# Optimization experiments

Measured on AMD Instinct MI355X. Metric: run time of the kernel, lower is better.

The kernel has to match this reference:

```python
import jax, jax.numpy as jnp
import numpy as np

N_NODES = 50000
N_EDGES = 800000
IN_DIM = 128
HIDDEN = 256
N_CLASSES = 10
N_GRAPHS = 64


def setup_inputs() -> dict:
    key = jax.random.key(0)
    ks = jax.random.split(key, 12)
    x = jax.random.normal(ks[0], (N_NODES, IN_DIM), dtype=jnp.float32)
    edge_index = jax.random.randint(ks[1], (2, N_EDGES), 0, N_NODES, dtype=jnp.int64)
    batch = jnp.sort(jax.random.randint(ks[2], (N_NODES,), 0, N_GRAPHS, dtype=jnp.int64))
    s = 1.0 / np.sqrt(IN_DIM)
    sh = 1.0 / np.sqrt(HIDDEN)
    return {
        "x": x,
        "edge_index": edge_index,
        "batch": batch,
        # layer 0 (in_dim -> hidden), weights stored [in, out]
        "Wg0": jax.random.uniform(ks[3], (IN_DIM, HIDDEN), jnp.float32, -s, s),
        "Wl0": jax.random.uniform(ks[4], (IN_DIM, HIDDEN), jnp.float32, -s, s),
        "Ws0": jax.random.uniform(ks[5], (IN_DIM, HIDDEN), jnp.float32, -s, s),
        "b0": jnp.zeros((HIDDEN,), jnp.float32),
        # layer 1 (hidden -> hidden)
        "Wg1": jax.random.uniform(ks[6], (HIDDEN, HIDDEN), jnp.float32, -sh, sh),
        "Wl1": jax.random.uniform(ks[7], (HIDDEN, HIDDEN), jnp.float32, -sh, sh),
        "Ws1": jax.random.uniform(ks[8], (HIDDEN, HIDDEN), jnp.float32, -sh, sh),
        "b1": jnp.zeros((HIDDEN,), jnp.float32),
        # classifier (hidden -> num_classes)
        "Wc": jax.random.uniform(ks[9], (HIDDEN, N_CLASSES), jnp.float32, -sh, sh),
        "bc": jax.random.uniform(ks[10], (N_CLASSES,), jnp.float32, -sh, sh),
    }


def _demo_layer(h, src, dst, deg, Wg, Wl, Ws, b):
    # global transform on all nodes
    g = h @ Wg
    # per-node mean of neighbor features over outgoing edges (== degree-bucket mean)
    neigh_sum = jax.ops.segment_sum(h[dst], src, num_segments=N_NODES)
    neigh_mean = neigh_sum / jnp.maximum(deg, 1.0)[:, None]
    # degree-0 nodes receive only the global branch (as in the torch loop)
    out = g + jnp.where((deg > 0)[:, None], neigh_mean @ Wl + h @ Ws, 0.0)
    return jax.nn.elu(out + b)  # dropout is identity in eval mode


def reference(x, edge_index, batch, Wg0, Wl0, Ws0, b0, Wg1, Wl1, Ws1, b1, Wc, bc):
    src, dst = edge_index[0], edge_index[1]
    deg = jax.ops.segment_sum(jnp.ones(src.shape[0], x.dtype), src, num_segments=N_NODES)
    h = _demo_layer(x, src, dst, deg, Wg0, Wl0, Ws0, b0)
    h = _demo_layer(h, src, dst, deg, Wg1, Wl1, Ws1, b1)
    # global mean pool per graph
    cnt = jax.ops.segment_sum(jnp.ones(N_NODES, h.dtype), batch, num_segments=N_GRAPHS)
    g = jax.ops.segment_sum(h, batch, num_segments=N_GRAPHS) / jnp.maximum(cnt, 1.0)[:, None]
    return g @ Wc + bc
```

## Files before the change

### kernel.cpp

```cpp
#include <hip/hip_runtime.h>

#define N_NODES 50000
#define N_PAD   50048
#define N_EDGES 800000
#define IN_DIM 128
#define HIDDEN 256
#define N_CLASSES 10
#define N_GRAPHS 64

#define SCAN_BLK 1024
#define NB_SCAN ((N_NODES + SCAN_BLK - 1) / SCAN_BLK)

typedef __attribute__((ext_vector_type(8))) short short8;
typedef __attribute__((ext_vector_type(4))) float f32x4;

__device__ __forceinline__ float bf2f(unsigned short h) {
    union { unsigned int u; float f; } v; v.u = ((unsigned int)h) << 16; return v.f;
}
__device__ __forceinline__ unsigned short f2bf(float f) {
    union { float f; unsigned int u; } v; v.f = f;
    unsigned int u = v.u;
    u += 0x7FFFu + ((u >> 16) & 1u);
    return (unsigned short)(u >> 16);
}

__global__ void deg_count_kernel(const int* __restrict__ src, int* __restrict__ deg) {
    int e = blockIdx.x * blockDim.x + threadIdx.x;
    if (e < N_EDGES) atomicAdd(&deg[src[e]], 1);
}

__global__ __launch_bounds__(SCAN_BLK)
void block_sum_kernel(const int* __restrict__ deg, int* __restrict__ blocksum) {
    __shared__ int red[SCAN_BLK / 64];
    int i = blockIdx.x * SCAN_BLK + threadIdx.x;
    int v = (i < N_NODES) ? deg[i] : 0;
    #pragma unroll
    for (int off = 32; off; off >>= 1) v += __shfl_down(v, off, 64);
    if ((threadIdx.x & 63) == 0) red[threadIdx.x >> 6] = v;
    __syncthreads();
    if (threadIdx.x < 64) {
        int s = (threadIdx.x < SCAN_BLK / 64) ? red[threadIdx.x] : 0;
        #pragma unroll
        for (int off = 8; off; off >>= 1) s += __shfl_down(s, off, 64);
        if (threadIdx.x == 0) blocksum[blockIdx.x] = s;
    }
}

__global__ void block_offset_kernel(const int* __restrict__ blocksum, int* __restrict__ blockoff) {
    int lane = threadIdx.x;
    int v = (lane < NB_SCAN) ? blocksum[lane] : 0;
    #pragma unroll
    for (int off = 1; off < 64; off <<= 1) {
        int t = __shfl_up(v, off, 64);
        if (lane >= off) v += t;
    }
    int ex = __shfl_up(v, 1, 64);
    if (lane == 0) ex = 0;
    if (lane < NB_SCAN) blockoff[lane] = ex;
}

__global__ __launch_bounds__(SCAN_BLK)
void scan_phase_c_kernel(const int* __restrict__ deg, const int* __restrict__ blockoff,
                         int* __restrict__ rowptr, int* __restrict__ cursor,
                         float* __restrict__ rdeg,
                         int* __restrict__ d0cnt, int* __restrict__ d0list) {
    __shared__ int buf[SCAN_BLK];
    int i = blockIdx.x * SCAN_BLK + threadIdx.x;
    int v = (i < N_NODES) ? deg[i] : 0;
    buf[threadIdx.x] = v;
    __syncthreads();
    #pragma unroll
    for (int off = 1; off < SCAN_BLK; off <<= 1) {
        int t = (threadIdx.x >= off) ? buf[threadIdx.x - off] : 0;
        __syncthreads();
        buf[threadIdx.x] += t;
        __syncthreads();
    }
    int incl = buf[threadIdx.x] + blockoff[blockIdx.x];
    if (i < N_NODES) {
        rowptr[i + 1] = incl;
        cursor[i] = incl - v;
        rdeg[i] = (v > 0) ? 1.0f / (float)v : 0.0f;
        if (v == 0) { int p = atomicAdd(d0cnt, 1); d0list[p] = i; }
        if (i == 0) rowptr[0] = 0;
    }
}

__global__ void csr_fill_kernel(const int* __restrict__ src, const int* __restrict__ dst,
                                int* __restrict__ cursor, int* __restrict__ csr) {
    int e = blockIdx.x * blockDim.x + threadIdx.x;
    if (e < N_EDGES) {
        int p = atomicAdd(&cursor[src[e]], 1);
        csr[p] = dst[e];
    }
}

__global__ void cvt_bf16_kernel(const float* __restrict__ in, unsigned short* __restrict__ out, int n4) {
    int i = blockIdx.x * blockDim.x + threadIdx.x;
    if (i >= n4) return;
    float4 v = reinterpret_cast<const float4*>(in)[i];
    ushort4 o;
    o.x = f2bf(v.x); o.y = f2bf(v.y); o.z = f2bf(v.z); o.w = f2bf(v.w);
    reinterpret_cast<ushort4*>(out)[i] = o;
}

template<int D>
__global__ void prep_w_kernel(const float* __restrict__ Wg, const float* __restrict__ Wl,
                              const float* __restrict__ Ws, unsigned short* __restrict__ Wt) {
    int i = blockIdx.x * blockDim.x + threadIdx.x;
    if (i >= 256 * 2 * D) return;
    int c = i / (2 * D), k = i % (2 * D);
    float v;
    if (k < D) v = Wg[(size_t)k * 256 + c] + Ws[(size_t)k * 256 + c];
    else       v = Wl[(size_t)(k - D) * 256 + c];
    Wt[i] = f2bf(v);
}

template<int D>
__global__ __launch_bounds__(256)
void gather_mean_kernel(const int* __restrict__ rowptr, const int* __restrict__ csr,
                        const float* __restrict__ rdeg,
                        const unsigned short* __restrict__ H, unsigned short* __restrict__ NS) {
    constexpr int LPR = D / 8;
    constexpr int EPW = 64 / LPR;
    int node = blockIdx.x * 4 + (threadIdx.x >> 6);
    if (node >= N_NODES) return;
    const int lane = threadIdx.x & 63;
    const int sub = lane / LPR;
    const int sl  = lane % LPR;
    const int lo = rowptr[node], hi = rowptr[node + 1];
    const uint4* H4 = reinterpret_cast<const uint4*>(H);
    float a0=0.f,a1=0.f,a2=0.f,a3=0.f,a4=0.f,a5=0.f,a6=0.f,a7=0.f;
#define ACC8(v)                                        \
    do {                                               \
        a0 += bf2f((v).x & 0xFFFF); a1 += bf2f((v).x >> 16); \
        a2 += bf2f((v).y & 0xFFFF); a3 += bf2f((v).y >> 16); \
        a4 += bf2f((v).z & 0xFFFF); a5 += bf2f((v).z >> 16); \
        a6 += bf2f((v).w & 0xFFFF); a7 += bf2f((v).w >> 16); \
    } while (0)
    int j = lo;
    for (; j + 4 * EPW <= hi; j += 4 * EPW) {
        int d0 = csr[j + 0 * EPW + sub];
        int d1 = csr[j + 1 * EPW + sub];
        int d2 = csr[j + 2 * EPW + sub];
        int d3 = csr[j + 3 * EPW + sub];
        uint4 v0 = H4[(size_t)d0 * LPR + sl];
        uint4 v1 = H4[(size_t)d1 * LPR + sl];
        uint4 v2 = H4[(size_t)d2 * LPR + sl];
        uint4 v3 = H4[(size_t)d3 * LPR + sl];
        ACC8(v0); ACC8(v1); ACC8(v2); ACC8(v3);
    }
    for (; j + sub < hi; j += EPW) {
        uint4 v0 = H4[(size_t)csr[j + sub] * LPR + sl];
        ACC8(v0);
    }
#undef ACC8
    #pragma unroll
    for (int off = LPR; off < 64; off <<= 1) {
        a0 += __shfl_xor(a0, off, 64);
        a1 += __shfl_xor(a1, off, 64);
        a2 += __shfl_xor(a2, off, 64);
        a3 += __shfl_xor(a3, off, 64);
        a4 += __shfl_xor(a4, off, 64);
        a5 += __shfl_xor(a5, off, 64);
        a6 += __shfl_xor(a6, off, 64);
        a7 += __shfl_xor(a7, off, 64);
    }
    if (sub == 0) {
        float r = rdeg[node];
        uint4 o;
        o.x = (unsigned int)f2bf(a0 * r) | ((unsigned int)f2bf(a1 * r) << 16);
        o.y = (unsigned int)f2bf(a2 * r) | ((unsigned int)f2bf(a3 * r) << 16);
        o.z = (unsigned int)f2bf(a4 * r) | ((unsigned int)f2bf(a5 * r) << 16);
        o.w = (unsigned int)f2bf(a6 * r) | ((unsigned int)f2bf(a7 * r) << 16);
        reinterpret_cast<uint4*>(NS)[(size_t)node * LPR + sl] = o;
    }
}

template<int D>
__global__ __launch_bounds__(512)
void gemm_mfma_kernel(const unsigned short* __restrict__ X, const unsigned short* __restrict__ NS,
                      const unsigned short* __restrict__ Wt, const float* __restrict__ bias,
                      unsigned short* __restrict__ OUT) {
    constexpr int KTOT = 2 * D;
    __shared__ __align__(16) unsigned short A_lds[128 * 64];
    __shared__ __align__(16) unsigned short B_lds[256 * 64];
    const int tid = threadIdx.x;
    const int lane = tid & 63;
    const int wid = tid >> 6;
    const int wm = wid >> 2, wn = wid & 3;
    const int rowbase = blockIdx.x * 128;

    f32x4 acc[4][4];
    #pragma unroll
    for (int i = 0; i < 4; ++i)
        #pragma unroll
        for (int j = 0; j < 4; ++j) acc[i][j] = (f32x4)0.0f;

    for (int kt = 0; kt < KTOT; kt += 64) {
        const unsigned short* Aseg = (kt < D) ? X : NS;
        const int kd0 = (kt < D) ? kt : kt - D;
        #pragma unroll
        for (int p = 0; p < 2; ++p) {
            int c = (p * 8 + wid) * 64 + lane;
            int row = c >> 3, sl = c & 7;
            int ss = sl ^ (row & 7);
            const unsigned short* g = Aseg + (size_t)(rowbase + row) * D + kd0 + ss * 8;
            unsigned short* l = &A_lds[(size_t)(p * 8 + wid) * 512];
            __builtin_amdgcn_global_load_lds((const __attribute__((address_space(1))) unsigned int*)g,
                                             (__attribute__((address_space(3))) unsigned int*)l, 16, 0, 0);
        }
        #pragma unroll
        for (int p = 0; p < 4; ++p) {
            int c = (p * 8 + wid) * 64 + lane;
            int br = c >> 3, sl = c & 7;
            int ss = sl ^ (br & 7);
            const unsigned short* g = Wt + (size_t)br * KTOT + kt + ss * 8;
            unsigned short* l = &B_lds[(size_t)(p * 8 + wid) * 512];
            __builtin_amdgcn_global_load_lds((const __attribute__((address_space(1))) unsigned int*)g,
                                             (__attribute__((address_space(3))) unsigned int*)l, 16, 0, 0);
        }
        __syncthreads();
        #pragma unroll
        for (int ks = 0; ks < 2; ++ks) {
            short8 a[4], b[4];
            int s = ks * 4 + (lane >> 4);
            #pragma unroll
            for (int f = 0; f < 4; ++f) {
                int row = wm * 64 + f * 16 + (lane & 15);
                a[f] = *reinterpret_cast<const short8*>(&A_lds[row * 64 + ((s ^ (row & 7)) << 3)]);
                int col = wn * 64 + f * 16 + (lane & 15);
                b[f] = *reinterpret_cast<const short8*>(&B_lds[col * 64 + ((s ^ (col & 7)) << 3)]);
            }
            #pragma unroll
            for (int fi = 0; fi < 4; ++fi)
                #pragma unroll
                for (int fj = 0; fj < 4; ++fj)
                    acc[fi][fj] = __builtin_amdgcn_mfma_f32_16x16x32_bf16(a[fi], b[fj], acc[fi][fj], 0, 0, 0);
        }
        __syncthreads();
    }

    float bv[4];
    #pragma unroll
    for (int fj = 0; fj < 4; ++fj) bv[fj] = bias[wn * 64 + fj * 16 + (lane & 15)];
    #pragma unroll
    for (int fi = 0; fi < 4; ++fi) {
        #pragma unroll
        for (int r = 0; r < 4; ++r) {
            int row = rowbase + wm * 64 + fi * 16 + (lane >> 4) * 4 + r;
            if (row < N_NODES) {
                #pragma unroll
                for (int fj = 0; fj < 4; ++fj) {
                    float z = acc[fi][fj][r] + bv[fj];
                    z = z > 0.f ? z : (expf(z) - 1.f);
                    OUT[(size_t)row * 256 + wn * 64 + fj * 16 + (lane & 15)] = f2bf(z);
                }
            }
        }
    }
}

template<typename T, int D>
__global__ void fixup_kernel(const int* __restrict__ cnt, const int* __restrict__ list,
                             const T* __restrict__ X,
                             const float* __restrict__ Wg, const float* __restrict__ bias,
                             unsigned short* __restrict__ OUT) {
    int c = threadIdx.x;
    int n = *cnt;
    for (int i = blockIdx.x; i < n; i += gridDim.x) {
        int row = list[i];
        float acc = bias[c];
        for (int k = 0; k < D; ++k) {
            float xv;
            if constexpr (sizeof(T) == 4) xv = ((const float*)X)[(size_t)row * D + k];
            else                          xv = bf2f(((const unsigned short*)X)[(size_t)row * D + k]);
            acc = fmaf(xv, Wg[(size_t)k * 256 + c], acc);
        }
        acc = acc > 0.f ? acc : (expf(acc) - 1.f);
        OUT[(size_t)row * 256 + c] = f2bf(acc);
    }
}

__global__ __launch_bounds__(256)
void pool_partial_kernel(const unsigned short* __restrict__ H, const int* __restrict__ batch,
                         float* __restrict__ pooled) {
    const int base = blockIdx.x * 64;
    const int t = threadIdx.x;
    float acc = 0.0f;
    int cur = batch[base];
    const int end = (base + 64 < N_NODES) ? base + 64 : N_NODES;
    for (int r = base; r < end; ++r) {
        int g = batch[r];
        if (g != cur) {
            atomicAdd(&pooled[cur * HIDDEN + t], acc);
            acc = 0.0f; cur = g;
        }
        acc += bf2f(H[(size_t)r * HIDDEN + t]);
    }
    atomicAdd(&pooled[cur * HIDDEN + t], acc);
}

__global__ void classify_kernel(const float* __restrict__ pooled, const int* __restrict__ batch,
                                const float* __restrict__ Wc, const float* __restrict__ bc,
                                float* __restrict__ out) {
    __shared__ int s_lo, s_hi;
    __shared__ float pl[HIDDEN];
    int g = blockIdx.x;
    if (threadIdx.x == 0) {
        int lo = 0, hi = N_NODES;
        while (lo < hi) { int m = (lo + hi) >> 1; if (batch[m] < g) lo = m + 1; else hi = m; }
        s_lo = lo;
        int lo2 = lo, hi2 = N_NODES;
        while (lo2 < hi2) { int m = (lo2 + hi2) >> 1; if (batch[m] < g + 1) lo2 = m + 1; else hi2 = m; }
        s_hi = lo2;
    }
    __syncthreads();
    int t = threadIdx.x;
    float cnt = (float)(s_hi - s_lo);
    pl[t] = pooled[g * HIDDEN + t] / fmaxf(cnt, 1.0f);
    __syncthreads();
    if (t < N_CLASSES) {
        float accv = bc[t];
        #pragma unroll 4
        for (int k = 0; k < HIDDEN; ++k) accv = fmaf(pl[k], Wc[k * N_CLASSES + t], accv);
        out[g * N_CLASSES + t] = accv;
    }
}

extern "C" void kernel_launch(void* const* d_in, const int* in_sizes, int n_in,
                              void* d_out, int out_size, void* d_ws, size_t ws_size,
                              hipStream_t stream) {
    const float* x    = (const float*)d_in[0];
    const int*   ei   = (const int*)d_in[1];
    const int*   batch= (const int*)d_in[2];
    const float* Wg0  = (const float*)d_in[3];
    const float* Wl0  = (const float*)d_in[4];
    const float* Ws0  = (const float*)d_in[5];
    const float* b0   = (const float*)d_in[6];
    const float* Wg1  = (const float*)d_in[7];
    const float* Wl1  = (const float*)d_in[8];
    const float* Ws1  = (const float*)d_in[9];
    const float* b1   = (const float*)d_in[10];
    const float* Wc   = (const float*)d_in[11];
    const float* bc   = (const float*)d_in[12];
    const int* src = ei;
    const int* dst = ei + N_EDGES;

    char* ws = (char*)d_ws;
    int*            deg    = (int*)(ws + 0);
    int*            d0cnt  = (int*)(ws + 200192);
    int*            blocksum = (int*)(ws + 200704);
    int*            blockoff = (int*)(ws + 201216);
    float*          rdeg   = (float*)(ws + 262144);
    int*            rowptr = (int*)(ws + 524288);
    int*            cursor = (int*)(ws + 786432);
    float*          pooled = (float*)(ws + 786432);
    int*            csr    = (int*)(ws + 1048576);
    int*            d0list = (int*)(ws + 4259840);
    unsigned short* x_bf   = (unsigned short*)(ws + 4521984);
    unsigned short* ns0_bf = (unsigned short*)(ws + 17334272);
    unsigned short* h1_bf  = (unsigned short*)(ws + 30146560);
    unsigned short* ns1_bf = (unsigned short*)(ws + 55771136);
    unsigned short* h2_bf  = (unsigned short*)(ws + 81395712);
    unsigned short* Wt0    = (unsigned short*)(ws + 107020288);
    unsigned short* Wt1    = (unsigned short*)(ws + 107151360);

    hipMemsetAsync(ws, 0, 262144, stream);

    deg_count_kernel<<<(N_EDGES + 255) / 256, 256, 0, stream>>>(src, deg);
    block_sum_kernel<<<NB_SCAN, SCAN_BLK, 0, stream>>>(deg, blocksum);
    block_offset_kernel<<<1, 64, 0, stream>>>(blocksum, blockoff);
    scan_phase_c_kernel<<<NB_SCAN, SCAN_BLK, 0, stream>>>(deg, blockoff, rowptr, cursor, rdeg, d0cnt, d0list);
    csr_fill_kernel<<<(N_EDGES + 255) / 256, 256, 0, stream>>>(src, dst, cursor, csr);

    prep_w_kernel<IN_DIM><<<(256 * 2 * IN_DIM + 255) / 256, 256, 0, stream>>>(Wg0, Wl0, Ws0, Wt0);
    prep_w_kernel<HIDDEN><<<(256 * 2 * HIDDEN + 255) / 256, 256, 0, stream>>>(Wg1, Wl1, Ws1, Wt1);
    cvt_bf16_kernel<<<(N_NODES * IN_DIM / 4 + 255) / 256, 256, 0, stream>>>(x, x_bf, N_NODES * IN_DIM / 4);

    gather_mean_kernel<IN_DIM><<<(N_NODES + 3) / 4, 256, 0, stream>>>(rowptr, csr, rdeg, x_bf, ns0_bf);
    gemm_mfma_kernel<IN_DIM><<<(N_NODES + 127) / 128, 512, 0, stream>>>(x_bf, ns0_bf, Wt0, b0, h1_bf);
    fixup_kernel<float, IN_DIM><<<64, 256, 0, stream>>>(d0cnt, d0list, x, Wg0, b0, h1_bf);

    gather_mean_kernel<HIDDEN><<<(N_NODES + 3) / 4, 256, 0, stream>>>(rowptr, csr, rdeg, h1_bf, ns1_bf);
    gemm_mfma_kernel<HIDDEN><<<(N_NODES + 127) / 128, 512, 0, stream>>>(h1_bf, ns1_bf, Wt1, b1, h2_bf);
    fixup_kernel<unsigned short, HIDDEN><<<64, 256, 0, stream>>>(d0cnt, d0list, h1_bf, Wg1, b1, h2_bf);

    hipMemsetAsync(pooled, 0, N_GRAPHS * HIDDEN * sizeof(float), stream);
    pool_partial_kernel<<<(N_NODES + 63) / 64, 256, 0, stream>>>(h2_bf, batch, pooled);
    classify_kernel<<<N_GRAPHS, HIDDEN, 0, stream>>>(pooled, batch, Wc, bc, (float*)d_out);
}
```

Baseline: 277.3 us.

## Fuse graph mean-pooling into layer-2 GEMM epilogue and merge prep kernels

The second-layer GEMM epilogue now applies bias and ELU and accumulates straight into per-graph pooled sums. It does a warp-level reduction when all 64 rows share a graph and falls back to per-element atomics otherwise. This removes writing the full bf16 h2 activation and the separate pooling pass that read it back. Degree-0 nodes are handled by a new fixup kernel that atomically adds the difference between the correct output and the value the GEMM already pooled. The input conversion and both weight-prep kernels are merged into one launch. The cost is more atomic traffic on the pooled buffer and a slightly riskier correction path.

```diff
diff --git a/kernel.cpp b/kernel.cpp
--- a/kernel.cpp
+++ b/kernel.cpp
@@ -95,25 +95,35 @@
     }
 }
 
-__global__ void cvt_bf16_kernel(const float* __restrict__ in, unsigned short* __restrict__ out, int n4) {
+#define N_CVT (N_NODES * IN_DIM / 4)
+__global__ void prep_all_kernel(const float* __restrict__ x, unsigned short* __restrict__ x_bf,
+                                const float* __restrict__ Wg0, const float* __restrict__ Wl0,
+                                const float* __restrict__ Ws0, unsigned short* __restrict__ Wt0,
+                                const float* __restrict__ Wg1, const float* __restrict__ Wl1,
+                                const float* __restrict__ Ws1, unsigned short* __restrict__ Wt1) {
     int i = blockIdx.x * blockDim.x + threadIdx.x;
-    if (i >= n4) return;
-    float4 v = reinterpret_cast<const float4*>(in)[i];
-    ushort4 o;
-    o.x = f2bf(v.x); o.y = f2bf(v.y); o.z = f2bf(v.z); o.w = f2bf(v.w);
-    reinterpret_cast<ushort4*>(out)[i] = o;
-}
-
-template<int D>
-__global__ void prep_w_kernel(const float* __restrict__ Wg, const float* __restrict__ Wl,
-                              const float* __restrict__ Ws, unsigned short* __restrict__ Wt) {
-    int i = blockIdx.x * blockDim.x + threadIdx.x;
-    if (i >= 256 * 2 * D) return;
-    int c = i / (2 * D), k = i % (2 * D);
-    float v;
-    if (k < D) v = Wg[(size_t)k * 256 + c] + Ws[(size_t)k * 256 + c];
-    else       v = Wl[(size_t)(k - D) * 256 + c];
-    Wt[i] = f2bf(v);
+    if (i < N_CVT) {
+        float4 v = reinterpret_cast<const float4*>(x)[i];
+        ushort4 o;
+        o.x = f2bf(v.x); o.y = f2bf(v.y); o.z = f2bf(v.z); o.w = f2bf(v.w);
+        reinterpret_cast<ushort4*>(x_bf)[i] = o;
+        return;
+    }
+    i -= N_CVT;
+    if (i < 256 * 2 * IN_DIM) {
+        int c = i / (2 * IN_DIM), k = i % (2 * IN_DIM);
+        float v = (k < IN_DIM) ? Wg0[(size_t)k * 256 + c] + Ws0[(size_t)k * 256 + c]
+                               : Wl0[(size_t)(k - IN_DIM) * 256 + c];
+        Wt0[i] = f2bf(v);
+        return;
+    }
+    i -= 256 * 2 * IN_DIM;
+    if (i < 256 * 2 * HIDDEN) {
+        int c = i / (2 * HIDDEN), k = i % (2 * HIDDEN);
+        float v = (k < HIDDEN) ? Wg1[(size_t)k * 256 + c] + Ws1[(size_t)k * 256 + c]
+                               : Wl1[(size_t)(k - HIDDEN) * 256 + c];
+        Wt1[i] = f2bf(v);
+    }
 }
 
 template<int D>
@@ -131,12 +141,12 @@
     const int lo = rowptr[node], hi = rowptr[node + 1];
     const uint4* H4 = reinterpret_cast<const uint4*>(H);
     float a0=0.f,a1=0.f,a2=0.f,a3=0.f,a4=0.f,a5=0.f,a6=0.f,a7=0.f;
-#define ACC8(v)                                        \
-    do {                                               \
-        a0 += bf2f((v).x & 0xFFFF); a1 += bf2f((v).x >> 16); \
-        a2 += bf2f((v).y & 0xFFFF); a3 += bf2f((v).y >> 16); \
-        a4 += bf2f((v).z & 0xFFFF); a5 += bf2f((v).z >> 16); \
-        a6 += bf2f((v).w & 0xFFFF); a7 += bf2f((v).w >> 16); \
+#define ACC8(vv)                                              \
+    do {                                                      \
+        a0 += bf2f((vv).x & 0xFFFF); a1 += bf2f((vv).x >> 16);\
+        a2 += bf2f((vv).y & 0xFFFF); a3 += bf2f((vv).y >> 16);\
+        a4 += bf2f((vv).z & 0xFFFF); a5 += bf2f((vv).z >> 16);\
+        a6 += bf2f((vv).w & 0xFFFF); a7 += bf2f((vv).w >> 16);\
     } while (0)
     int j = lo;
     for (; j + 4 * EPW <= hi; j += 4 * EPW) {
@@ -177,10 +187,11 @@
     }
 }
 
-template<int D>
+template<int D, bool POOL>
 __global__ __launch_bounds__(512)
 void gemm_mfma_kernel(const unsigned short* __restrict__ X, const unsigned short* __restrict__ NS,
                       const unsigned short* __restrict__ Wt, const float* __restrict__ bias,
+                      const int* __restrict__ batch, float* __restrict__ pooled,
                       unsigned short* __restrict__ OUT) {
     constexpr int KTOT = 2 * D;
     __shared__ __align__(16) unsigned short A_lds[128 * 64];
@@ -244,26 +255,78 @@
     float bv[4];
     #pragma unroll
     for (int fj = 0; fj < 4; ++fj) bv[fj] = bias[wn * 64 + fj * 16 + (lane & 15)];
-    #pragma unroll
-    for (int fi = 0; fi < 4; ++fi) {
-        #pragma unroll
-        for (int r = 0; r < 4; ++r) {
-            int row = rowbase + wm * 64 + fi * 16 + (lane >> 4) * 4 + r;
-            if (row < N_NODES) {
-                #pragma unroll
-                for (int fj = 0; fj < 4; ++fj) {
-                    float z = acc[fi][fj][r] + bv[fj];
-                    z = z > 0.f ? z : (expf(z) - 1.f);
-                    OUT[(size_t)row * 256 + wn * 64 + fj * 16 + (lane & 15)] = f2bf(z);
+
+    if (!POOL) {
+        #pragma unroll
+        for (int fi = 0; fi < 4; ++fi) {
+            #pragma unroll
+            for (int r = 0; r < 4; ++r) {
+                int row = rowbase + wm * 64 + fi * 16 + (lane >> 4) * 4 + r;
+                if (row < N_NODES) {
+                    #pragma unroll
+                    for (int fj = 0; fj < 4; ++fj) {
+                        float z = acc[fi][fj][r] + bv[fj];
+                        z = z > 0.f ? z : (expf(z) - 1.f);
+                        OUT[(size_t)row * 256 + wn * 64 + fj * 16 + (lane & 15)] = f2bf(z);
+                    }
                 }
             }
         }
-    }
-}
-
-template<typename T, int D>
+    } else {
+        const int wrow0 = rowbase + wm * 64;
+        const int wrow63 = wrow0 + 63;
+        bool fast = (wrow63 < N_NODES) && (batch[wrow0] == batch[wrow63]);
+        if (fast) {
+            int g = batch[wrow0];
+            float s0 = 0.f, s1 = 0.f, s2 = 0.f, s3 = 0.f;
+            #pragma unroll
+            for (int fi = 0; fi < 4; ++fi) {
+                #pragma unroll
+                for (int r = 0; r < 4; ++r) {
+                    float z0 = acc[fi][0][r] + bv[0];
+                    float z1 = acc[fi][1][r] + bv[1];
+                    float z2 = acc[fi][2][r] + bv[2];
+                    float z3 = acc[fi][3][r] + bv[3];
+                    s0 += z0 > 0.f ? z0 : (expf(z0) - 1.f);
+                    s1 += z1 > 0.f ? z1 : (expf(z1) - 1.f);
+                    s2 += z2 > 0.f ? z2 : (expf(z2) - 1.f);
+                    s3 += z3 > 0.f ? z3 : (expf(z3) - 1.f);
+                }
+            }
+            s0 += __shfl_xor(s0, 16, 64); s0 += __shfl_xor(s0, 32, 64);
+            s1 += __shfl_xor(s1, 16, 64); s1 += __shfl_xor(s1, 32, 64);
+            s2 += __shfl_xor(s2, 16, 64); s2 += __shfl_xor(s2, 32, 64);
+            s3 += __shfl_xor(s3, 16, 64); s3 += __shfl_xor(s3, 32, 64);
+            if (lane < 16) {
+                float* pg = pooled + (size_t)g * 256 + wn * 64 + lane;
+                atomicAdd(pg + 0,  s0);
+                atomicAdd(pg + 16, s1);
+                atomicAdd(pg + 32, s2);
+                atomicAdd(pg + 48, s3);
+            }
+        } else {
+            #pragma unroll
+            for (int fi = 0; fi < 4; ++fi) {
+                #pragma unroll
+                for (int r = 0; r < 4; ++r) {
+                    int row = rowbase + wm * 64 + fi * 16 + (lane >> 4) * 4 + r;
+                    if (row < N_NODES) {
+                        int g = batch[row];
+                        #pragma unroll
+                        for (int fj = 0; fj < 4; ++fj) {
+                            float z = acc[fi][fj][r] + bv[fj];
+                            z = z > 0.f ? z : (expf(z) - 1.f);
+                            atomicAdd(&pooled[(size_t)g * 256 + wn * 64 + fj * 16 + (lane & 15)], z);
+                        }
+                    }
+                }
+            }
+        }
+    }
+}
+
 __global__ void fixup_kernel(const int* __restrict__ cnt, const int* __restrict__ list,
-                             const T* __restrict__ X,
+                             const float* __restrict__ X,
                              const float* __restrict__ Wg, const float* __restrict__ bias,
                              unsigned short* __restrict__ OUT) {
     int c = threadIdx.x;
@@ -271,34 +334,33 @@
     for (int i = blockIdx.x; i < n; i += gridDim.x) {
         int row = list[i];
         float acc = bias[c];
-        for (int k = 0; k < D; ++k) {
-            float xv;
-            if constexpr (sizeof(T) == 4) xv = ((const float*)X)[(size_t)row * D + k];
-            else                          xv = bf2f(((const unsigned short*)X)[(size_t)row * D + k]);
-            acc = fmaf(xv, Wg[(size_t)k * 256 + c], acc);
-        }
+        for (int k = 0; k < IN_DIM; ++k)
+            acc = fmaf(X[(size_t)row * IN_DIM + k], Wg[(size_t)k * 256 + c], acc);
         acc = acc > 0.f ? acc : (expf(acc) - 1.f);
         OUT[(size_t)row * 256 + c] = f2bf(acc);
     }
 }
 
-__global__ __launch_bounds__(256)
-void pool_partial_kernel(const unsigned short* __restrict__ H, const int* __restrict__ batch,
-                         float* __restrict__ pooled) {
-    const int base = blockIdx.x * 64;
-    const int t = threadIdx.x;
-    float acc = 0.0f;
-    int cur = batch[base];
-    const int end = (base + 64 < N_NODES) ? base + 64 : N_NODES;
-    for (int r = base; r < end; ++r) {
-        int g = batch[r];
-        if (g != cur) {
-            atomicAdd(&pooled[cur * HIDDEN + t], acc);
-            acc = 0.0f; cur = g;
-        }
-        acc += bf2f(H[(size_t)r * HIDDEN + t]);
-    }
-    atomicAdd(&pooled[cur * HIDDEN + t], acc);
+__global__ void fixup_pool_kernel(const int* __restrict__ cnt, const int* __restrict__ list,
+                                  const unsigned short* __restrict__ X,
+                                  const float* __restrict__ Wg, const float* __restrict__ Ws,
+                                  const float* __restrict__ bias,
+                                  const int* __restrict__ batch, float* __restrict__ pooled) {
+    int c = threadIdx.x;
+    int n = *cnt;
+    for (int i = blockIdx.x; i < n; i += gridDim.x) {
+        int row = list[i];
+        float ag = bias[c], as = 0.f;
+        for (int k = 0; k < HIDDEN; ++k) {
+            float xv = bf2f(X[(size_t)row * HIDDEN + k]);
+            ag = fmaf(xv, Wg[(size_t)k * 256 + c], ag);
+            as = fmaf(xv, Ws[(size_t)k * 256 + c], as);
+        }
+        float correct = ag > 0.f ? ag : (expf(ag) - 1.f);
+        float zw = ag + as;
+        float wrong = zw > 0.f ? zw : (expf(zw) - 1.f);
+        atomicAdd(&pooled[(size_t)batch[row] * 256 + c], correct - wrong);
+    }
 }
 
 __global__ void classify_kernel(const float* __restrict__ pooled, const int* __restrict__ batch,
@@ -362,7 +424,6 @@
     unsigned short* ns0_bf = (unsigned short*)(ws + 17334272);
     unsigned short* h1_bf  = (unsigned short*)(ws + 30146560);
     unsigned short* ns1_bf = (unsigned short*)(ws + 55771136);
-    unsigned short* h2_bf  = (unsigned short*)(ws + 81395712);
     unsigned short* Wt0    = (unsigned short*)(ws + 107020288);
     unsigned short* Wt1    = (unsigned short*)(ws + 107151360);
 
@@ -374,19 +435,23 @@
     scan_phase_c_kernel<<<NB_SCAN, SCAN_BLK, 0, stream>>>(deg, blockoff, rowptr, cursor, rdeg, d0cnt, d0list);
     csr_fill_kernel<<<(N_EDGES + 255) / 256, 256, 0, stream>>>(src, dst, cursor, csr);
 
-    prep_w_kernel<IN_DIM><<<(256 * 2 * IN_DIM + 255) / 256, 256, 0, stream>>>(Wg0, Wl0, Ws0, Wt0);
-    prep_w_kernel<HIDDEN><<<(256 * 2 * HIDDEN + 255) / 256, 256, 0, stream>>>(Wg1, Wl1, Ws1, Wt1);
-    cvt_bf16_kernel<<<(N_NODES * IN_DIM / 4 + 255) / 256, 256, 0, stream>>>(x, x_bf, N_NODES * IN_DIM / 4);
+    hipMemsetAsync(pooled, 0, N_GRAPHS * HIDDEN * sizeof(float), stream);
+
+    {
+        int total = N_CVT + 256 * 2 * IN_DIM + 256 * 2 * HIDDEN;
+        prep_all_kernel<<<(total + 255) / 256, 256, 0, stream>>>(
+            x, x_bf, Wg0, Wl0, Ws0, Wt0, Wg1, Wl1, Ws1, Wt1);
+    }
 
     gather_mean_kernel<IN_DIM><<<(N_NODES + 3) / 4, 256, 0, stream>>>(rowptr, csr, rdeg, x_bf, ns0_bf);
-    gemm_mfma_kernel<IN_DIM><<<(N_NODES + 127) / 128, 512, 0, stream>>>(x_bf, ns0_bf, Wt0, b0, h1_bf);
-    fixup_kernel<float, IN_DIM><<<64, 256, 0, stream>>>(d0cnt, d0list, x, Wg0, b0, h1_bf);
+    gemm_mfma_kernel<IN_DIM, false><<<(N_NODES + 127) / 128, 512, 0, stream>>>(
+        x_bf, ns0_bf, Wt0, b0, batch, pooled, h1_bf);
+    fixup_kernel<<<64, 256, 0, stream>>>(d0cnt, d0list, x, Wg0, b0, h1_bf);
 
     gather_mean_kernel<HIDDEN><<<(N_NODES + 3) / 4, 256, 0, stream>>>(rowptr, csr, rdeg, h1_bf, ns1_bf);
-    gemm_mfma_kernel<HIDDEN><<<(N_NODES + 127) / 128, 512, 0, stream>>>(h1_bf, ns1_bf, Wt1, b1, h2_bf);
-    fixup_kernel<unsigned short, HIDDEN><<<64, 256, 0, stream>>>(d0cnt, d0list, h1_bf, Wg1, b1, h2_bf);
-
-    hipMemsetAsync(pooled, 0, N_GRAPHS * HIDDEN * sizeof(float), stream);
-    pool_partial_kernel<<<(N_NODES + 63) / 64, 256, 0, stream>>>(h2_bf, batch, pooled);
+    gemm_mfma_kernel<HIDDEN, true><<<(N_NODES + 127) / 128, 512, 0, stream>>>(
+        h1_bf, ns1_bf, Wt1, b1, batch, pooled, nullptr);
+    fixup_pool_kernel<<<64, 256, 0, stream>>>(d0cnt, d0list, h1_bf, Wg1, Ws1, b1, batch, pooled);
+
     classify_kernel<<<N_GRAPHS, HIDDEN, 0, stream>>>(pooled, batch, Wc, bc, (float*)d_out);
 }
```

Result: no change. 280.0 us (+1.0%).
